# Optimization experiments

Measured on AMD Instinct MI355X. Metric: run time of the kernel, lower is better.

Reference implementation:

```python
import jax, jax.numpy as jnp
import numpy as np

B, T, D, H, L = 16384, 100, 5, 32, 1  # batch, seq_len, input/output dim, hidden, latent


def setup_inputs() -> dict:
    key = jax.random.key(0)
    ks = jax.random.split(key, 28)
    rn = lambda k, shp, s=0.1: jax.random.normal(k, shp, dtype=jnp.float32) * s
    return {
        "x": rn(ks[0], (B, T, D), 1.0),
        "eps": rn(ks[1], (B, L), 1.0),
        # Encoder LSTM (PyTorch layout: W_ih [4H, D], W_hh [4H, H], gate order i,f,g,o)
        "enc_Wih": rn(ks[2], (4 * H, D)), "enc_Whh": rn(ks[3], (4 * H, H)),
        "enc_bih": rn(ks[4], (4 * H,)), "enc_bhh": rn(ks[5], (4 * H,)),
        "W_mu": rn(ks[6], (L, 2 * H)), "b_mu": rn(ks[7], (L,)),
        "W_lv": rn(ks[8], (L, 2 * H)), "b_lv": rn(ks[9], (L,)),
        # Decoder
        "W_l2h": rn(ks[10], (H, L)), "b_l2h": rn(ks[11], (H,)),
        "W_l2h2": rn(ks[12], (H, L)), "b_l2h2": rn(ks[13], (H,)),
        "start_token": jnp.zeros((1, D), jnp.float32),
        "W_emb": rn(ks[14], (H, D)), "b_emb": rn(ks[15], (H,)),
        "dec_Wih": rn(ks[16], (4 * H, H)), "dec_Whh": rn(ks[17], (4 * H, H)),
        "dec_bih": rn(ks[18], (4 * H,)), "dec_bhh": rn(ks[19], (4 * H,)),
        "W_out": rn(ks[20], (D, H)), "b_out": rn(ks[21], (D,)),
        "W_seq": rn(ks[22], (H, L)), "b_seq": rn(ks[23], (H,)),
        "W_seq2": rn(ks[24], (1, H)), "b_seq2": rn(ks[25], (1,)),
    }


def _lstm_cell(x_t, h, c, Wih, Whh, b):
    g = x_t @ Wih.T + h @ Whh.T + b            # [B, 4H]
    i, f, gg, o = jnp.split(g, 4, axis=-1)      # PyTorch gate order i,f,g,o
    c = jax.nn.sigmoid(f) * c + jax.nn.sigmoid(i) * jnp.tanh(gg)
    h = jax.nn.sigmoid(o) * jnp.tanh(c)
    return h, c


def reference(x, eps, enc_Wih, enc_Whh, enc_bih, enc_bhh, W_mu, b_mu, W_lv, b_lv,
              W_l2h, b_l2h, W_l2h2, b_l2h2, start_token, W_emb, b_emb,
              dec_Wih, dec_Whh, dec_bih, dec_bhh, W_out, b_out,
              W_seq, b_seq, W_seq2, b_seq2):
    bsz, seq_len, _ = x.shape
    hdim = enc_Whh.shape[1]
    lrelu = lambda v: jax.nn.leaky_relu(v, negative_slope=0.01)

    # ---- Encoder LSTM over time ----
    b_enc = enc_bih + enc_bhh
    def enc_step(carry, x_t):
        h, c = carry
        h, c = _lstm_cell(x_t, h, c, enc_Wih, enc_Whh, b_enc)
        return (h, c), None
    z0 = jnp.zeros((bsz, hdim), x.dtype)
    (h_n, c_n), _ = jax.lax.scan(enc_step, (z0, z0), jnp.swapaxes(x, 0, 1))
    hcat = jnp.concatenate([h_n, c_n], axis=-1)        # [B, 2H]
    mu = hcat @ W_mu.T + b_mu                           # [B, L]
    log_var = hcat @ W_lv.T + b_lv                      # [B, L]

    # ---- Reparameterize ----
    z = mu + eps * jnp.exp(0.5 * log_var)

    h0 = lrelu(mu @ W_l2h.T + b_l2h)                    # [B, H]
    c0 = lrelu(mu @ W_l2h2.T + b_l2h2)                  # [B, H]
    x0 = jnp.broadcast_to(start_token @ W_emb.T + b_emb, (bsz, hdim))
    b_dec = dec_bih + dec_bhh
    def dec_step(carry, _):
        x_in, h, c = carry
        x_t = jax.nn.relu(x_in)
        h, c = _lstm_cell(x_t, h, c, dec_Wih, dec_Whh, b_dec)
        return (h, h, c), h
    _, hs = jax.lax.scan(dec_step, (x0, h0, c0), None, length=seq_len)  # [T, B, H]
    recon = jnp.swapaxes(hs, 0, 1) @ W_out.T + b_out    # [B, T, D]

    # ---- num head on z (encoder_outputs arg) ----
    num = jax.nn.relu(lrelu(z @ W_seq.T + b_seq) @ W_seq2.T + b_seq2)  # [B, 1]

    return recon, mu, log_var, num
```

## Files before the change

kernel.cpp:

```cpp
#include <hip/hip_runtime.h>
#include <hip/hip_bf16.h>

typedef short bf16x8 __attribute__((ext_vector_type(8)));
typedef float f32x4  __attribute__((ext_vector_type(4)));
typedef unsigned int u32x4 __attribute__((ext_vector_type(4)));

#define LOG2E 1.44269504088896340736f

static __device__ __forceinline__ unsigned short f2bf(float f){
    __hip_bfloat16 h = __float2bfloat16(f);
    return __builtin_bit_cast(unsigned short, h);
}
static __device__ __forceinline__ float bf2f(unsigned short u){
    unsigned v = ((unsigned)u) << 16;
    return __builtin_bit_cast(float, v);
}
static __device__ __forceinline__ unsigned pk_bf16(float lo, float hi){
    return (((unsigned)f2bf(hi)) << 16) | (unsigned)f2bf(lo);
}
static __device__ __forceinline__ float rcp_(float x){ return __builtin_amdgcn_rcpf(x); }
static __device__ __forceinline__ float ex2(float x){ return __builtin_amdgcn_exp2f(x); }
static __device__ __forceinline__ void lds_fence(){
    asm volatile("s_waitcnt lgkmcnt(0)" ::: "memory");
}
static __device__ __forceinline__ f32x4 mfma16(bf16x8 a, bf16x8 b, f32x4 c){
    return __builtin_amdgcn_mfma_f32_16x16x32_bf16(a, b, c, 0, 0, 0);
}

__global__ void marker_kernel(float* out, int n, float v){
    int i = blockIdx.x * 256 + threadIdx.x;
    if (i < n) out[i] = v;
}

__global__ __launch_bounds__(256, 1)
void vae_mfma2_kernel(const float* __restrict__ x,      const float* __restrict__ eps,
                      const float* __restrict__ eWih,   const float* __restrict__ eWhh,
                      const float* __restrict__ ebih,   const float* __restrict__ ebhh,
                      const float* __restrict__ Wmu,    const float* __restrict__ bmu,
                      const float* __restrict__ Wlv,    const float* __restrict__ blv,
                      const float* __restrict__ Wl2h,   const float* __restrict__ bl2h,
                      const float* __restrict__ Wl2h2,  const float* __restrict__ bl2h2,
                      const float* __restrict__ stok,   const float* __restrict__ Wemb,
                      const float* __restrict__ bemb,
                      const float* __restrict__ dWih,   const float* __restrict__ dWhh,
                      const float* __restrict__ dbih,   const float* __restrict__ dbhh,
                      const float* __restrict__ Wout,   const float* __restrict__ bout,
                      const float* __restrict__ Wseq,   const float* __restrict__ bseq,
                      const float* __restrict__ Wseq2,  const float* __restrict__ bseq2,
                      float* __restrict__ recon,
                      float* __restrict__ out_mu,
                      float* __restrict__ out_lv,
                      float* __restrict__ out_num)
{
    __shared__ unsigned hb[4][16][20];
    __shared__ float cbuf[4][16][36];
    __shared__ float mubuf[4][16];
    __shared__ float x0buf[4][32];
    __shared__ float cw[524];

    const int tid = threadIdx.x;
    const int w   = tid >> 6;
    const int l   = tid & 63;
    const int c   = l & 15;
    const int g   = l >> 4;
    const int bbase = blockIdx.x * 64 + w * 16;

    if (tid < 64){ cw[tid] = Wmu[tid]; cw[64+tid] = Wlv[tid]; }
    if (tid < 32){
        cw[128+tid] = Wseq[tid];  cw[160+tid] = bseq[tid];  cw[192+tid] = Wseq2[tid];
        cw[224+tid] = Wl2h[tid];  cw[256+tid] = bl2h[tid];
        cw[288+tid] = Wl2h2[tid]; cw[320+tid] = bl2h2[tid];
    }
    if (tid < 160) cw[352+tid] = Wout[tid];
    if (tid < 5)   cw[512+tid] = bout[tid];
    if (tid == 0){ cw[517] = bmu[0]; cw[518] = blv[0]; cw[519] = bseq2[0]; }
    __syncthreads();

    bf16x8 BW[8], BX[8];
    f32x4  biasv[8];
    #pragma unroll
    for (int n=0;n<8;++n){
        const int row = (n>>1)*32 + 2*c + (n&1);
        const float sc = (n==4||n==5) ? (-2.0f*LOG2E) : (-LOG2E);
        bf16x8 t;
        #pragma unroll
        for (int j=0;j<8;++j) t[j] = (short)f2bf(sc * eWhh[(size_t)row*32 + g*8 + j]);
        BW[n] = t;
        bf16x8 tx = (bf16x8)0;
        if (g == 0){
            #pragma unroll
            for (int j=0;j<5;++j) tx[j] = (short)f2bf(sc * eWih[(size_t)row*5 + j]);
        }
        BX[n] = tx;
        float bv = sc * (ebih[row] + ebhh[row]);
        f32x4 b4; b4[0]=b4[1]=b4[2]=b4[3]=bv;
        biasv[n] = b4;
    }

    float cs[8];
    #pragma unroll
    for (int k=0;k<8;++k) cs[k] = 0.0f;
    #pragma unroll
    for (int q=0;q<4;++q) hb[w][g*4+q][c] = 0u;
    lds_fence();

    float4 xA = {0,0,0,0}; float xB = 0.0f;
    if (g == 0){
        const float* xp = x + (size_t)(bbase+c)*500;
        xA = *(const float4*)xp; xB = xp[4];
    }

    for (int t=0; t<100; ++t){
        bf16x8 ax = (bf16x8)0;
        if (g == 0){
            ax[0]=(short)f2bf(xA.x); ax[1]=(short)f2bf(xA.y);
            ax[2]=(short)f2bf(xA.z); ax[3]=(short)f2bf(xA.w);
            ax[4]=(short)f2bf(xB);
            if (t < 99){
                const float* xp = x + (size_t)(bbase+c)*500 + (t+1)*5;
                xA = *(const float4*)xp; xB = xp[4];
            }
        }
        u32x4 av = *(const u32x4*)&hb[w][c][g*4];
        bf16x8 ah = __builtin_bit_cast(bf16x8, av);

        f32x4 acc[8];
        #pragma unroll
        for (int n=0;n<8;++n){
            f32x4 a = mfma16(ax, BX[n], biasv[n]);
            acc[n] = mfma16(ah, BW[n], a);
        }

        #pragma unroll
        for (int q=0;q<4;++q){
            float hpair[2];
            #pragma unroll
            for (int u=0;u<2;++u){
                float ei = ex2(acc[0+u][q]);
                float ef = ex2(acc[2+u][q]);
                float eg = ex2(acc[4+u][q]);
                float eo = ex2(acc[6+u][q]);
                float pig = (1.0f+ei)*(1.0f+eg);
                float num = cs[u*4+q]*pig + (1.0f+ef)*(1.0f-eg);
                float cn  = num * rcp_((1.0f+ef)*pig);
                float ec  = ex2(cn * (-2.0f*LOG2E));
                hpair[u]  = (1.0f-ec) * rcp_((1.0f+eo)*(1.0f+ec));
                cs[u*4+q] = cn;
            }
            hb[w][g*4+q][c] = pk_bf16(hpair[0], hpair[1]);
        }
        lds_fence();
    }

    #pragma unroll
    for (int q=0;q<4;++q){
        cbuf[w][g*4+q][2*c]   = cs[q];
        cbuf[w][g*4+q][2*c+1] = cs[4+q];
    }
    lds_fence();

    bf16x8 BI[8], BH[8];
    f32x4  dbias[8];
    #pragma unroll
    for (int n=0;n<8;++n){
        const int row = (n>>1)*32 + 2*c + (n&1);
        const float sc = (n==4||n==5) ? (-2.0f*LOG2E) : (-LOG2E);
        bf16x8 ti, th;
        #pragma unroll
        for (int j=0;j<8;++j){
            ti[j] = (short)f2bf(sc * dWih[(size_t)row*32 + g*8 + j]);
            th[j] = (short)f2bf(sc * dWhh[(size_t)row*32 + g*8 + j]);
        }
        BI[n] = ti; BH[n] = th;
        float bv = sc * (dbih[row] + dbhh[row]);
        f32x4 b4; b4[0]=b4[1]=b4[2]=b4[3]=bv;
        dbias[n] = b4;
    }
    bf16x8 BO = (bf16x8)0;
    f32x4 bosv; bosv[0]=bosv[1]=bosv[2]=bosv[3]=0.0f;
    if (c < 5){
        bf16x8 to;
        #pragma unroll
        for (int j=0;j<8;++j) to[j] = (short)f2bf(Wout[c*32 + g*8 + j]);
        BO = to;
        float b = bout[c];
        bosv[0]=bosv[1]=bosv[2]=bosv[3]=b;
    }

    if (l < 16){
        const int r = l;
        const unsigned short* hrow = (const unsigned short*)&hb[w][r][0];
        float mu = cw[517], lv = cw[518];
        #pragma unroll
        for (int k=0;k<32;++k){
            float hvv = bf2f(hrow[k]);
            float cvv = cbuf[w][r][k];
            mu += hvv*cw[k]    + cvv*cw[32+k];
            lv += hvv*cw[64+k] + cvv*cw[96+k];
        }
        out_mu[bbase+r] = mu;
        out_lv[bbase+r] = lv;
        mubuf[w][r] = mu;
        float z = mu + eps[bbase+r] * __builtin_amdgcn_exp2f(0.5f*LOG2E*lv);
        float a2 = cw[519];
        #pragma unroll
        for (int j=0;j<32;++j){
            float s = z*cw[128+j] + cw[160+j];
            s = s > 0.0f ? s : 0.01f*s;
            a2 += cw[192+j]*s;
        }
        out_num[bbase+r] = fmaxf(a2, 0.0f);
    }
    if (l < 32){
        float v = bemb[l];
        #pragma unroll
        for (int d=0; d<5; ++d) v += stok[d]*Wemb[l*5 + d];
        x0buf[w][l] = fmaxf(v, 0.0f);
    }
    lds_fence();

    #pragma unroll
    for (int q=0;q<4;++q){
        const int row = g*4 + q;
        float muv = mubuf[w][row];
        float a0 = muv*cw[224+2*c]   + cw[256+2*c];
        float a1 = muv*cw[224+2*c+1] + cw[256+2*c+1];
        a0 = a0 > 0.0f ? a0 : 0.01f*a0;
        a1 = a1 > 0.0f ? a1 : 0.01f*a1;
        hb[w][row][c] = pk_bf16(a0, a1);
        float b0 = muv*cw[288+2*c]   + cw[320+2*c];
        float b1 = muv*cw[288+2*c+1] + cw[320+2*c+1];
        cs[q]   = b0 > 0.0f ? b0 : 0.01f*b0;
        cs[4+q] = b1 > 0.0f ? b1 : 0.01f*b1;
    }
    lds_fence();

    bf16x8 ax0;
    #pragma unroll
    for (int j=0;j<8;++j) ax0[j] = (short)f2bf(x0buf[w][g*8 + j]);

    for (int t=0; t<100; ++t){
        u32x4 av = *(const u32x4*)&hb[w][c][g*4];
        bf16x8 ah = __builtin_bit_cast(bf16x8, av);

        u32x4 rv;
        #pragma unroll
        for (int i=0;i<4;++i){
            unsigned v = av[i];
            unsigned m = ((v >> 15) & 0x00010001u) * 0xFFFFu;
            rv[i] = v & ~m;
        }
        bf16x8 ar = __builtin_bit_cast(bf16x8, rv);

        if (t > 0){
            f32x4 ao = mfma16(ah, BO, bosv);
            if (c < 5){
                #pragma unroll
                for (int q=0;q<4;++q)
                    recon[(size_t)(bbase + g*4 + q)*500 + (t-1)*5 + c] = ao[q];
            }
        }

        bf16x8 ax = (t == 0) ? ax0 : ar;

        f32x4 acc[8];
        #pragma unroll
        for (int n=0;n<8;++n){
            f32x4 a = mfma16(ax, BI[n], dbias[n]);
            acc[n] = mfma16(ah, BH[n], a);
        }

        #pragma unroll
        for (int q=0;q<4;++q){
            float hpair[2];
            #pragma unroll
            for (int u=0;u<2;++u){
                float ei = ex2(acc[0+u][q]);
                float ef = ex2(acc[2+u][q]);
                float eg = ex2(acc[4+u][q]);
                float eo = ex2(acc[6+u][q]);
                float pig = (1.0f+ei)*(1.0f+eg);
                float num = cs[u*4+q]*pig + (1.0f+ef)*(1.0f-eg);
                float cn  = num * rcp_((1.0f+ef)*pig);
                float ec  = ex2(cn * (-2.0f*LOG2E));
                hpair[u]  = (1.0f-ec) * rcp_((1.0f+eo)*(1.0f+ec));
                cs[u*4+q] = cn;
            }
            hb[w][g*4+q][c] = pk_bf16(hpair[0], hpair[1]);
        }
        lds_fence();
    }

    {
        u32x4 av = *(const u32x4*)&hb[w][c][g*4];
        bf16x8 ah = __builtin_bit_cast(bf16x8, av);
        f32x4 ao = mfma16(ah, BO, bosv);
        if (c < 5){
            #pragma unroll
            for (int q=0;q<4;++q)
                recon[(size_t)(bbase + g*4 + q)*500 + 99*5 + c] = ao[q];
        }
    }
}

extern "C" void kernel_launch(void* const* d_in, const int* in_sizes, int n_in,
                              void* d_out, int out_size, void* d_ws, size_t ws_size,
                              hipStream_t stream)
{
    (void)d_ws; (void)ws_size;
    static const int EXPECT[27] = {8192000,16384,640,4096,128,128,64,1,64,1,
                                   32,32,32,32,5,160,32,4096,4096,128,128,
                                   160,5,32,32,32,1};
    bool in_ok = (n_in == 27);
    if (in_ok) for (int i = 0; i < 27; ++i) in_ok = in_ok && (in_sizes[i] == EXPECT[i]);
    bool out_ok = (out_size == 8241152);

    float* out = (float*)d_out;
    if (!in_ok){
        marker_kernel<<<(out_size + 255)/256, 256, 0, stream>>>(out, out_size, 2.0f);
        return;
    }
    if (!out_ok){
        marker_kernel<<<(out_size + 255)/256, 256, 0, stream>>>(out, out_size, 3.0f);
        return;
    }

    const float* x     = (const float*)d_in[0];
    const float* eps   = (const float*)d_in[1];
    const float* eWih  = (const float*)d_in[2];
    const float* eWhh  = (const float*)d_in[3];
    const float* ebih  = (const float*)d_in[4];
    const float* ebhh  = (const float*)d_in[5];
    const float* Wmu   = (const float*)d_in[6];
    const float* bmu   = (const float*)d_in[7];
    const float* Wlv   = (const float*)d_in[8];
    const float* blv   = (const float*)d_in[9];
    const float* Wl2h  = (const float*)d_in[10];
    const float* bl2h  = (const float*)d_in[11];
    const float* Wl2h2 = (const float*)d_in[12];
    const float* bl2h2 = (const float*)d_in[13];
    const float* stok  = (const float*)d_in[14];
    const float* Wemb  = (const float*)d_in[15];
    const float* bemb  = (const float*)d_in[16];
    const float* dWih  = (const float*)d_in[17];
    const float* dWhh  = (const float*)d_in[18];
    const float* dbih  = (const float*)d_in[19];
    const float* dbhh  = (const float*)d_in[20];
    const float* Wout  = (const float*)d_in[21];
    const float* bout  = (const float*)d_in[22];
    const float* Wseq  = (const float*)d_in[23];
    const float* bseq  = (const float*)d_in[24];
    const float* Wseq2 = (const float*)d_in[25];
    const float* bseq2 = (const float*)d_in[26];

    float* recon  = out;
    float* out_mu = out + 8192000;
    float* out_lv = out_mu + 16384;
    float* out_nm = out_lv + 16384;

    vae_mfma2_kernel<<<256, 256, 0, stream>>>(x, eps,
        eWih, eWhh, ebih, ebhh, Wmu, bmu, Wlv, blv,
        Wl2h, bl2h, Wl2h2, bl2h2, stok, Wemb, bemb,
        dWih, dWhh, dbih, dbhh, Wout, bout,
        Wseq, bseq, Wseq2, bseq2,
        recon, out_mu, out_lv, out_nm);
}
```

Measured before the change: 154.5 us.

## Swap MFMA operand roles so LSTM hidden state stays in registers

Transposes the recurrent MFMA formulation: weights become the A operand and the hidden state the B operand, with gate rows permuted so each lane's output accumulator holds exactly the hidden units it needs as the next step's B input. This removes the per-timestep LDS write of h, the lgkmcnt fence and the LDS reload from both the encoder and decoder loops, keeping the recurrence entirely in registers. The recon output projection is transposed too, so each lane writes contiguous features of one batch row. LDS is now used only at the encoder/decoder handoff, with fp32 h/c buffers.

```diff
diff --git a/kernel.cpp b/kernel.cpp
--- a/kernel.cpp
+++ b/kernel.cpp
@@ -33,7 +33,7 @@
 }
 
 __global__ __launch_bounds__(256, 1)
-void vae_mfma2_kernel(const float* __restrict__ x,      const float* __restrict__ eps,
+void vae_mfma3_kernel(const float* __restrict__ x,      const float* __restrict__ eps,
                       const float* __restrict__ eWih,   const float* __restrict__ eWhh,
                       const float* __restrict__ ebih,   const float* __restrict__ ebhh,
                       const float* __restrict__ Wmu,    const float* __restrict__ bmu,
@@ -52,8 +52,8 @@
                       float* __restrict__ out_lv,
                       float* __restrict__ out_num)
 {
-    __shared__ unsigned hb[4][16][20];
-    __shared__ float cbuf[4][16][36];
+    __shared__ float hbf[4][16][33];
+    __shared__ float cbf[4][16][33];
     __shared__ float mubuf[4][16];
     __shared__ float x0buf[4][32];
     __shared__ float cw[524];
@@ -76,33 +76,36 @@
     if (tid == 0){ cw[517] = bmu[0]; cw[518] = blv[0]; cw[519] = bseq2[0]; }
     __syncthreads();
 
-    bf16x8 BW[8], BX[8];
+    bf16x8 WH[8], WX[8];
     f32x4  biasv[8];
     #pragma unroll
     for (int n=0;n<8;++n){
-        const int row = (n>>1)*32 + 2*c + (n&1);
-        const float sc = (n==4||n==5) ? (-2.0f*LOG2E) : (-LOG2E);
+        const int gt = n>>1, half = n&1;
+        const float sc = (gt==2) ? (-2.0f*LOG2E) : (-LOG2E);
+        const int GRc = gt*32 + ((c>>2)<<3) + half*4 + (c&3);
         bf16x8 t;
         #pragma unroll
-        for (int j=0;j<8;++j) t[j] = (short)f2bf(sc * eWhh[(size_t)row*32 + g*8 + j]);
-        BW[n] = t;
+        for (int j=0;j<8;++j) t[j] = (short)f2bf(sc * eWhh[(size_t)GRc*32 + g*8 + j]);
+        WH[n] = t;
         bf16x8 tx = (bf16x8)0;
         if (g == 0){
             #pragma unroll
-            for (int j=0;j<5;++j) tx[j] = (short)f2bf(sc * eWih[(size_t)row*5 + j]);
-        }
-        BX[n] = tx;
-        float bv = sc * (ebih[row] + ebhh[row]);
-        f32x4 b4; b4[0]=b4[1]=b4[2]=b4[3]=bv;
+            for (int j=0;j<5;++j) tx[j] = (short)f2bf(sc * eWih[(size_t)GRc*5 + j]);
+        }
+        WX[n] = tx;
+        f32x4 b4;
+        #pragma unroll
+        for (int q=0;q<4;++q){
+            const int R = gt*32 + g*8 + half*4 + q;
+            b4[q] = sc * (ebih[R] + ebhh[R]);
+        }
         biasv[n] = b4;
     }
 
-    float cs[8];
-    #pragma unroll
-    for (int k=0;k<8;++k) cs[k] = 0.0f;
-    #pragma unroll
-    for (int q=0;q<4;++q) hb[w][g*4+q][c] = 0u;
-    lds_fence();
+    float cs[8], hn[8];
+    #pragma unroll
+    for (int k=0;k<8;++k){ cs[k] = 0.0f; hn[k] = 0.0f; }
+    u32x4 hpk = (u32x4)0;
 
     float4 xA = {0,0,0,0}; float xB = 0.0f;
     if (g == 0){
@@ -111,90 +114,97 @@
     }
 
     for (int t=0; t<100; ++t){
-        bf16x8 ax = (bf16x8)0;
+        bf16x8 bx = (bf16x8)0;
         if (g == 0){
-            ax[0]=(short)f2bf(xA.x); ax[1]=(short)f2bf(xA.y);
-            ax[2]=(short)f2bf(xA.z); ax[3]=(short)f2bf(xA.w);
-            ax[4]=(short)f2bf(xB);
+            bx[0]=(short)f2bf(xA.x); bx[1]=(short)f2bf(xA.y);
+            bx[2]=(short)f2bf(xA.z); bx[3]=(short)f2bf(xA.w);
+            bx[4]=(short)f2bf(xB);
             if (t < 99){
                 const float* xp = x + (size_t)(bbase+c)*500 + (t+1)*5;
                 xA = *(const float4*)xp; xB = xp[4];
             }
         }
-        u32x4 av = *(const u32x4*)&hb[w][c][g*4];
-        bf16x8 ah = __builtin_bit_cast(bf16x8, av);
+        bf16x8 bh = __builtin_bit_cast(bf16x8, hpk);
 
         f32x4 acc[8];
         #pragma unroll
         for (int n=0;n<8;++n){
-            f32x4 a = mfma16(ax, BX[n], biasv[n]);
-            acc[n] = mfma16(ah, BW[n], a);
+            f32x4 a = mfma16(WX[n], bx, biasv[n]);
+            acc[n] = mfma16(WH[n], bh, a);
         }
 
         #pragma unroll
         for (int q=0;q<4;++q){
-            float hpair[2];
-            #pragma unroll
-            for (int u=0;u<2;++u){
-                float ei = ex2(acc[0+u][q]);
-                float ef = ex2(acc[2+u][q]);
-                float eg = ex2(acc[4+u][q]);
-                float eo = ex2(acc[6+u][q]);
-                float pig = (1.0f+ei)*(1.0f+eg);
-                float num = cs[u*4+q]*pig + (1.0f+ef)*(1.0f-eg);
-                float cn  = num * rcp_((1.0f+ef)*pig);
-                float ec  = ex2(cn * (-2.0f*LOG2E));
-                hpair[u]  = (1.0f-ec) * rcp_((1.0f+eo)*(1.0f+ec));
-                cs[u*4+q] = cn;
-            }
-            hb[w][g*4+q][c] = pk_bf16(hpair[0], hpair[1]);
-        }
-        lds_fence();
-    }
-
-    #pragma unroll
-    for (int q=0;q<4;++q){
-        cbuf[w][g*4+q][2*c]   = cs[q];
-        cbuf[w][g*4+q][2*c+1] = cs[4+q];
+          #pragma unroll
+          for (int u=0;u<2;++u){
+            const int ul = u*4 + q;
+            float ei = ex2(acc[0+u][q]);
+            float ef = ex2(acc[2+u][q]);
+            float eg = ex2(acc[4+u][q]);
+            float eo = ex2(acc[6+u][q]);
+            float pig = (1.0f+ei)*(1.0f+eg);
+            float num = cs[ul]*pig + (1.0f+ef)*(1.0f-eg);
+            float cn  = num * rcp_((1.0f+ef)*pig);
+            float ec  = ex2(cn * (-2.0f*LOG2E));
+            hn[ul]    = (1.0f-ec) * rcp_((1.0f+eo)*(1.0f+ec));
+            cs[ul]    = cn;
+          }
+        }
+        hpk[0] = pk_bf16(hn[0], hn[1]);
+        hpk[1] = pk_bf16(hn[2], hn[3]);
+        hpk[2] = pk_bf16(hn[4], hn[5]);
+        hpk[3] = pk_bf16(hn[6], hn[7]);
+    }
+
+    #pragma unroll
+    for (int ul=0; ul<8; ++ul){
+        hbf[w][c][g*8+ul] = hn[ul];
+        cbf[w][c][g*8+ul] = cs[ul];
     }
     lds_fence();
 
-    bf16x8 BI[8], BH[8];
+    bf16x8 WI[8], WHd[8];
     f32x4  dbias[8];
     #pragma unroll
     for (int n=0;n<8;++n){
-        const int row = (n>>1)*32 + 2*c + (n&1);
-        const float sc = (n==4||n==5) ? (-2.0f*LOG2E) : (-LOG2E);
+        const int gt = n>>1, half = n&1;
+        const float sc = (gt==2) ? (-2.0f*LOG2E) : (-LOG2E);
+        const int GRc = gt*32 + ((c>>2)<<3) + half*4 + (c&3);
         bf16x8 ti, th;
         #pragma unroll
         for (int j=0;j<8;++j){
-            ti[j] = (short)f2bf(sc * dWih[(size_t)row*32 + g*8 + j]);
-            th[j] = (short)f2bf(sc * dWhh[(size_t)row*32 + g*8 + j]);
-        }
-        BI[n] = ti; BH[n] = th;
-        float bv = sc * (dbih[row] + dbhh[row]);
-        f32x4 b4; b4[0]=b4[1]=b4[2]=b4[3]=bv;
+            ti[j] = (short)f2bf(sc * dWih[(size_t)GRc*32 + g*8 + j]);
+            th[j] = (short)f2bf(sc * dWhh[(size_t)GRc*32 + g*8 + j]);
+        }
+        WI[n] = ti; WHd[n] = th;
+        f32x4 b4;
+        #pragma unroll
+        for (int q=0;q<4;++q){
+            const int R = gt*32 + g*8 + half*4 + q;
+            b4[q] = sc * (dbih[R] + dbhh[R]);
+        }
         dbias[n] = b4;
     }
-    bf16x8 BO = (bf16x8)0;
-    f32x4 bosv; bosv[0]=bosv[1]=bosv[2]=bosv[3]=0.0f;
+    bf16x8 WO = (bf16x8)0;
+    f32x4 bosv = (f32x4)0;
     if (c < 5){
         bf16x8 to;
         #pragma unroll
         for (int j=0;j<8;++j) to[j] = (short)f2bf(Wout[c*32 + g*8 + j]);
-        BO = to;
-        float b = bout[c];
-        bosv[0]=bosv[1]=bosv[2]=bosv[3]=b;
+        WO = to;
+    }
+    #pragma unroll
+    for (int q=0;q<4;++q){
+        const int dd = g*4 + q;
+        bosv[q] = (dd < 5) ? bout[dd] : 0.0f;
     }
 
     if (l < 16){
         const int r = l;
-        const unsigned short* hrow = (const unsigned short*)&hb[w][r][0];
         float mu = cw[517], lv = cw[518];
         #pragma unroll
         for (int k=0;k<32;++k){
-            float hvv = bf2f(hrow[k]);
-            float cvv = cbuf[w][r][k];
+            float hvv = hbf[w][r][k], cvv = cbf[w][r][k];
             mu += hvv*cw[k]    + cvv*cw[32+k];
             lv += hvv*cw[64+k] + cvv*cw[96+k];
         }
@@ -219,87 +229,84 @@
     }
     lds_fence();
 
-    #pragma unroll
-    for (int q=0;q<4;++q){
-        const int row = g*4 + q;
-        float muv = mubuf[w][row];
-        float a0 = muv*cw[224+2*c]   + cw[256+2*c];
-        float a1 = muv*cw[224+2*c+1] + cw[256+2*c+1];
-        a0 = a0 > 0.0f ? a0 : 0.01f*a0;
-        a1 = a1 > 0.0f ? a1 : 0.01f*a1;
-        hb[w][row][c] = pk_bf16(a0, a1);
-        float b0 = muv*cw[288+2*c]   + cw[320+2*c];
-        float b1 = muv*cw[288+2*c+1] + cw[320+2*c+1];
-        cs[q]   = b0 > 0.0f ? b0 : 0.01f*b0;
-        cs[4+q] = b1 > 0.0f ? b1 : 0.01f*b1;
-    }
-    lds_fence();
-
-    bf16x8 ax0;
-    #pragma unroll
-    for (int j=0;j<8;++j) ax0[j] = (short)f2bf(x0buf[w][g*8 + j]);
+    {
+        const float muv = mubuf[w][c];
+        #pragma unroll
+        for (int ul=0; ul<8; ++ul){
+            const int U = g*8 + ul;
+            float a = muv*cw[224+U] + cw[256+U];
+            float b = muv*cw[288+U] + cw[320+U];
+            hn[ul] = (a > 0.0f ? a : 0.01f*a);
+            cs[ul] = (b > 0.0f ? b : 0.01f*b);
+        }
+        hpk[0] = pk_bf16(hn[0], hn[1]);
+        hpk[1] = pk_bf16(hn[2], hn[3]);
+        hpk[2] = pk_bf16(hn[4], hn[5]);
+        hpk[3] = pk_bf16(hn[6], hn[7]);
+    }
+    bf16x8 bx0;
+    #pragma unroll
+    for (int j=0;j<8;++j) bx0[j] = (short)f2bf(x0buf[w][g*8 + j]);
 
     for (int t=0; t<100; ++t){
-        u32x4 av = *(const u32x4*)&hb[w][c][g*4];
-        bf16x8 ah = __builtin_bit_cast(bf16x8, av);
-
-        u32x4 rv;
-        #pragma unroll
-        for (int i=0;i<4;++i){
-            unsigned v = av[i];
-            unsigned m = ((v >> 15) & 0x00010001u) * 0xFFFFu;
-            rv[i] = v & ~m;
-        }
-        bf16x8 ar = __builtin_bit_cast(bf16x8, rv);
+        bf16x8 bh = __builtin_bit_cast(bf16x8, hpk);
 
         if (t > 0){
-            f32x4 ao = mfma16(ah, BO, bosv);
-            if (c < 5){
-                #pragma unroll
-                for (int q=0;q<4;++q)
-                    recon[(size_t)(bbase + g*4 + q)*500 + (t-1)*5 + c] = ao[q];
+            f32x4 ao = mfma16(WO, bh, bosv);
+            float* rp = recon + (size_t)(bbase+c)*500 + (t-1)*5;
+            if (g == 0){ rp[0]=ao[0]; rp[1]=ao[1]; rp[2]=ao[2]; rp[3]=ao[3]; }
+            else if (g == 1){ rp[4]=ao[0]; }
+        }
+
+        bf16x8 bx;
+        if (t == 0) bx = bx0;
+        else {
+            u32x4 rv;
+            #pragma unroll
+            for (int i=0;i<4;++i){
+                unsigned v = hpk[i];
+                unsigned m = ((v >> 15) & 0x00010001u) * 0xFFFFu;
+                rv[i] = v & ~m;
             }
-        }
-
-        bf16x8 ax = (t == 0) ? ax0 : ar;
+            bx = __builtin_bit_cast(bf16x8, rv);
+        }
 
         f32x4 acc[8];
         #pragma unroll
         for (int n=0;n<8;++n){
-            f32x4 a = mfma16(ax, BI[n], dbias[n]);
-            acc[n] = mfma16(ah, BH[n], a);
+            f32x4 a = mfma16(WI[n], bx, dbias[n]);
+            acc[n] = mfma16(WHd[n], bh, a);
         }
 
         #pragma unroll
         for (int q=0;q<4;++q){
-            float hpair[2];
-            #pragma unroll
-            for (int u=0;u<2;++u){
-                float ei = ex2(acc[0+u][q]);
-                float ef = ex2(acc[2+u][q]);
-                float eg = ex2(acc[4+u][q]);
-                float eo = ex2(acc[6+u][q]);
-                float pig = (1.0f+ei)*(1.0f+eg);
-                float num = cs[u*4+q]*pig + (1.0f+ef)*(1.0f-eg);
-                float cn  = num * rcp_((1.0f+ef)*pig);
-                float ec  = ex2(cn * (-2.0f*LOG2E));
-                hpair[u]  = (1.0f-ec) * rcp_((1.0f+eo)*(1.0f+ec));
-                cs[u*4+q] = cn;
-            }
-            hb[w][g*4+q][c] = pk_bf16(hpair[0], hpair[1]);
-        }
-        lds_fence();
+          #pragma unroll
+          for (int u=0;u<2;++u){
+            const int ul = u*4 + q;
+            float ei = ex2(acc[0+u][q]);
+            float ef = ex2(acc[2+u][q]);
+            float eg = ex2(acc[4+u][q]);
+            float eo = ex2(acc[6+u][q]);
+            float pig = (1.0f+ei)*(1.0f+eg);
+            float num = cs[ul]*pig + (1.0f+ef)*(1.0f-eg);
+            float cn  = num * rcp_((1.0f+ef)*pig);
+            float ec  = ex2(cn * (-2.0f*LOG2E));
+            hn[ul]    = (1.0f-ec) * rcp_((1.0f+eo)*(1.0f+ec));
+            cs[ul]    = cn;
+          }
+        }
+        hpk[0] = pk_bf16(hn[0], hn[1]);
+        hpk[1] = pk_bf16(hn[2], hn[3]);
+        hpk[2] = pk_bf16(hn[4], hn[5]);
+        hpk[3] = pk_bf16(hn[6], hn[7]);
     }
 
     {
-        u32x4 av = *(const u32x4*)&hb[w][c][g*4];
-        bf16x8 ah = __builtin_bit_cast(bf16x8, av);
-        f32x4 ao = mfma16(ah, BO, bosv);
-        if (c < 5){
-            #pragma unroll
-            for (int q=0;q<4;++q)
-                recon[(size_t)(bbase + g*4 + q)*500 + 99*5 + c] = ao[q];
-        }
+        bf16x8 bh = __builtin_bit_cast(bf16x8, hpk);
+        f32x4 ao = mfma16(WO, bh, bosv);
+        float* rp = recon + (size_t)(bbase+c)*500 + 99*5;
+        if (g == 0){ rp[0]=ao[0]; rp[1]=ao[1]; rp[2]=ao[2]; rp[3]=ao[3]; }
+        else if (g == 1){ rp[4]=ao[0]; }
     }
 }
 
@@ -358,7 +365,7 @@
     float* out_lv = out_mu + 16384;
     float* out_nm = out_lv + 16384;
 
-    vae_mfma2_kernel<<<256, 256, 0, stream>>>(x, eps,
+    vae_mfma3_kernel<<<256, 256, 0, stream>>>(x, eps,
         eWih, eWhh, ebih, ebhh, Wmu, bmu, Wlv, blv,
         Wl2h, bl2h, Wl2h2, bl2h2, stok, Wemb, bemb,
         dWih, dWhh, dbih, dbhh, Wout, bout,
```

New measurement: 136.9 us. 1.13x faster.
